# Kernel tuning notes

Hardware: AMD Instinct MI355X
Metric: run time of the kernel (lower is better)

Reference implementation:

```python
import jax, jax.numpy as jnp
import numpy as np

WS = (2, 7, 7)       # window size (d,h,w)
SS = (1, 3, 3)       # shift size
NH = 6               # num heads
EPS = 1e-5


def _layernorm(x, g, b):
    m = jnp.mean(x, axis=-1, keepdims=True)
    v = jnp.mean((x - m) ** 2, axis=-1, keepdims=True)
    return (x - m) * jax.lax.rsqrt(v + EPS) * g + b


def _window_partition(x, ws):
    # x: (B, D, H, W, C) -> (B*nW, N, C)
    B, D, H, W, C = x.shape
    x = x.reshape(B, D // ws[0], ws[0], H // ws[1], ws[1], W // ws[2], ws[2], C)
    x = x.transpose(0, 1, 3, 5, 2, 4, 6, 7)
    return x.reshape(-1, ws[0] * ws[1] * ws[2], C)


def _window_reverse(w, ws, B, D, H, W):
    # w: (B*nW, N, C) -> (B, D, H, W, C)
    C = w.shape[-1]
    x = w.reshape(B, D // ws[0], H // ws[1], W // ws[2], ws[0], ws[1], ws[2], C)
    x = x.transpose(0, 1, 4, 2, 5, 3, 6, 7)
    return x.reshape(B, D, H, W, C)


def _rel_pos_index(ws):
    coords = np.stack(np.meshgrid(np.arange(ws[0]), np.arange(ws[1]), np.arange(ws[2]), indexing='ij'))
    cf = coords.reshape(3, -1)                      # (3, N)
    rel = cf[:, :, None] - cf[:, None, :]           # (3, N, N)
    rel = rel.transpose(1, 2, 0).copy()             # (N, N, 3)
    rel[..., 0] += ws[0] - 1
    rel[..., 1] += ws[1] - 1
    rel[..., 2] += ws[2] - 1
    rel[..., 0] *= (2 * ws[1] - 1) * (2 * ws[2] - 1)
    rel[..., 1] *= 2 * ws[2] - 1
    return rel.sum(-1)                              # (N, N) int


def _compute_mask(Dp, Hp, Wp, ws, ss):
    img = np.zeros((1, Dp, Hp, Wp, 1), np.float32)
    cnt = 0
    for d in (slice(-ws[0]), slice(-ws[0], -ss[0]), slice(-ss[0], None)):
        for h in (slice(-ws[1]), slice(-ws[1], -ss[1]), slice(-ss[1], None)):
            for w in (slice(-ws[2]), slice(-ws[2], -ss[2]), slice(-ss[2], None)):
                img[:, d, h, w, :] = cnt
                cnt += 1
    mw = np.asarray(_window_partition(jnp.asarray(img), ws)).squeeze(-1)  # (nW, N)
    am = mw[:, None, :] - mw[:, :, None]
    return np.where(am != 0, -100.0, 0.0).astype(np.float32)


def setup_inputs() -> dict:
    key = jax.random.key(0)
    ks = jax.random.split(key, 8)
    B, D, H, W, C = 4, 8, 56, 56, 192
    hid = 4 * C
    tbl = (2 * WS[0] - 1) * (2 * WS[1] - 1) * (2 * WS[2] - 1)
    s = 0.02
    return {
        'x': jax.random.normal(ks[0], (B, D, H, W, C), jnp.float32),
        'mask_matrix': jnp.asarray(_compute_mask(D, H, W, WS, SS)),
        'norm1_g': jnp.ones((C,), jnp.float32),
        'norm1_b': jnp.zeros((C,), jnp.float32),
        'qkv_w': jax.random.normal(ks[1], (3 * C, C), jnp.float32) * s,
        'qkv_b': jnp.zeros((3 * C,), jnp.float32),
        'rpb_table': jax.random.normal(ks[2], (tbl, NH), jnp.float32) * s,
        'proj_w': jax.random.normal(ks[3], (C, C), jnp.float32) * s,
        'proj_b': jnp.zeros((C,), jnp.float32),
        'norm2_g': jnp.ones((C,), jnp.float32),
        'norm2_b': jnp.zeros((C,), jnp.float32),
        'fc1_w': jax.random.normal(ks[4], (hid, C), jnp.float32) * s,
        'fc1_b': jnp.zeros((hid,), jnp.float32),
        'fc2_w': jax.random.normal(ks[5], (C, hid), jnp.float32) * s,
        'fc2_b': jnp.zeros((C,), jnp.float32),
    }


def reference(x, mask_matrix, norm1_g, norm1_b, qkv_w, qkv_b, rpb_table,
              proj_w, proj_b, norm2_g, norm2_b, fc1_w, fc1_b, fc2_w, fc2_b):
    B, D, H, W, C = x.shape
    hd = C // NH
    scale = hd ** -0.5
    N = WS[0] * WS[1] * WS[2]
    rpi = _rel_pos_index(WS)  # constant (N, N)

    shortcut = x
    h = _layernorm(x, norm1_g, norm1_b)
    # cyclic shift (dims divisible by window, no padding needed)
    sx = jnp.roll(h, (-SS[0], -SS[1], -SS[2]), axis=(1, 2, 3))
    xw = _window_partition(sx, WS)                      # (B_, N, C)
    B_ = xw.shape[0]

    qkv = (xw @ qkv_w.T + qkv_b).reshape(B_, N, 3, NH, hd).transpose(2, 0, 3, 1, 4)
    q, k, v = qkv[0] * scale, qkv[1], qkv[2]            # (B_, NH, N, hd)
    attn = jnp.einsum('bhnd,bhmd->bhnm', q, k)          # (B_, NH, N, N)

    bias = rpb_table[rpi.reshape(-1)].reshape(N, N, NH).transpose(2, 0, 1)
    attn = attn + bias[None]

    nW = mask_matrix.shape[0]
    attn = attn.reshape(B_ // nW, nW, NH, N, N) + mask_matrix[None, :, None]
    attn = jax.nn.softmax(attn.reshape(B_, NH, N, N), axis=-1)

    out = jnp.einsum('bhnm,bhmd->bhnd', attn, v).swapaxes(1, 2).reshape(B_, N, C)
    out = out @ proj_w.T + proj_b

    sx = _window_reverse(out, WS, B, D, H, W)
    x1 = jnp.roll(sx, (SS[0], SS[1], SS[2]), axis=(1, 2, 3))

    x = shortcut + x1
    h2 = _layernorm(x, norm2_g, norm2_b)
    h2 = jax.nn.gelu(h2 @ fc1_w.T + fc1_b, approximate=False) @ fc2_w.T + fc2_b
    return x + h2
```

## Files before the change

kernel.cpp:

```cpp
#include <hip/hip_runtime.h>
#include <math.h>

typedef short short8 __attribute__((ext_vector_type(8)));
typedef __bf16 bf16x8 __attribute__((ext_vector_type(8)));
typedef float floatx4 __attribute__((ext_vector_type(4)));
typedef float f32x4 __attribute__((ext_vector_type(4)));
typedef unsigned short ushort;
typedef unsigned int uint;

#define NTOK 100352
#define CCH 192
#define NWIN 1024
#define NSEQ 98
#define NSEQP 112
#define NHEAD 6
#define HD 32
#define VSTR 136
#define PSTR 40

typedef const __attribute__((address_space(1))) uint guint_t;
typedef __attribute__((address_space(3))) uint luint_t;

__device__ __forceinline__ float bf2f(ushort u) {
    union { uint i; float f; } x; x.i = ((uint)u) << 16; return x.f;
}
__device__ __forceinline__ ushort f2bf(float f) {
    uint u = __float_as_uint(f);
    uint r = (u + 0x7FFFu + ((u >> 16) & 1u)) >> 16;
    return (ushort)r;
}
__device__ __forceinline__ uint pack2bf(float a, float b) {
    return (uint)f2bf(a) | ((uint)f2bf(b) << 16);
}
__device__ __forceinline__ float ldT(const void* p, size_t i, bool bf) {
    return bf ? bf2f(((const ushort*)p)[i]) : ((const float*)p)[i];
}

__global__ void detect_kernel(const uint* __restrict__ n1g, uint* __restrict__ flag) {
    if (threadIdx.x == 0) flag[0] = (n1g[0] == 0x3F800000u) ? 0u : 1u;
}

__global__ __launch_bounds__(256) void prepw_kernel(
    const void* __restrict__ src, ushort* __restrict__ dst,
    int K, int NT, const void* __restrict__ g,
    const uint* __restrict__ flagp, int total)
{
    const bool bf = (*flagp != 0u);
    int e = blockIdx.x * 256 + threadIdx.x;
    if (e >= total) return;
    int j = e / K, kk = e - j * K;
    int nt = j >> 6, r = j & 63;
    int kc = kk / 192; int k2 = kk - kc * 192;
    int ktc = k2 >> 5, c = k2 & 31;
    int ci = kc * (NT * 6) + nt * 6 + ktc;
    int byteoff = (ci << 12) + (((r << 6) + (c << 1)) ^ ((r & 7) << 4));
    float vv = ldT(src, e, bf);
    if (g) vv *= ldT(g, kk, bf);
    *(ushort*)((char*)dst + byteoff) = f2bf(vv);
}

__global__ __launch_bounds__(256) void prepmisc_kernel(
    const void* qkvb, const void* projb, const void* fc2b,
    const void* fc1b, const void* fc1w, const void* g2, const void* b2,
    float* __restrict__ FB, const uint* __restrict__ flagp)
{
    const bool bf = (*flagp != 0u);
    int j = blockIdx.x * 256 + threadIdx.x;
    if (j >= 768) return;
    if (j < 576) FB[j] = ldT(qkvb, j, bf);
    if (j < 192) { FB[576 + j] = ldT(projb, j, bf); FB[768 + j] = ldT(fc2b, j, bf); }
    float c1 = 0.f, c2 = 0.f;
    for (int kk = 0; kk < 192; ++kk) {
        float w = ldT(fc1w, (size_t)j * 192 + kk, bf);
        c1 = fmaf(w, ldT(g2, kk, bf), c1);
        c2 = fmaf(w, ldT(b2, kk, bf), c2);
    }
    FB[1728 + j] = c1;
    FB[960 + j]  = c2 + ldT(fc1b, j, bf);
}

__global__ __launch_bounds__(256) void prepTB_kernel(
    const void* __restrict__ rpb, const void* __restrict__ mask,
    float* __restrict__ TB, const uint* __restrict__ flagp)
{
    const bool bf = (*flagp != 0u);
    int i = blockIdx.x * 256 + threadIdx.x;
    if (i >= 8 * NHEAD * 7 * NSEQP * 16) return;
    int ky16 = i & 15; int t1 = i >> 4;
    int qy = t1 % NSEQP; int t2 = t1 / NSEQP;
    int kt = t2 % 7; int t3 = t2 / 7;
    int head = t3 % NHEAD; int combo = t3 / NHEAD;
    int ky = kt * 16 + ky16;
    int kcl = ky < 97 ? ky : 97, qcl = qy < 97 ? qy : 97;
    int md = kcl / 49, mr = kcl % 49; int mh = mr / 7, mw = mr % 7;
    int nd = qcl / 49, nr = qcl % 49; int nh = nr / 7, nw = nr % 7;
    int idx = (nd - md) * 169 + (nh - mh) * 13 + (nw - mw) + 253;
    float b = ldT(rpb, (size_t)idx * NHEAD + head, bf);
    int wrem = ((combo & 4) ? (3 << 6) : 0) | ((combo & 2) ? (7 << 3) : 0) | ((combo & 1) ? 7 : 0);
    float m = ldT(mask, (size_t)wrem * (NSEQ * NSEQ) + (size_t)kcl * NSEQ + qcl, bf);
    TB[i] = b + m;
}

__global__ __launch_bounds__(256) void ln1_kernel(
    const void* __restrict__ x, const void* __restrict__ g,
    const void* __restrict__ b, ushort* __restrict__ xw,
    const uint* __restrict__ flagp)
{
    const bool bf = (*flagp != 0u);
    int tid = blockIdx.x * 4 + (threadIdx.x >> 6);
    int lane = threadIdx.x & 63;
    int wi = tid / NSEQ, n = tid % NSEQ;
    int bb = wi >> 8; int rem = wi & 255;
    int wd = rem >> 6; int wh = (rem >> 3) & 7; int ww = rem & 7;
    int dz = n / 49; int r2 = n % 49; int hy = r2 / 7; int wx = r2 % 7;
    int dd = wd * 2 + dz, hh = wh * 7 + hy, w2 = ww * 7 + wx;
    int dsrc = (dd + 1) & 7;
    int hsrc = hh + 3; if (hsrc >= 56) hsrc -= 56;
    int wsrc = w2 + 3; if (wsrc >= 56) wsrc -= 56;
    size_t base = ((size_t)((bb * 8 + dsrc) * 56 + hsrc) * 56 + wsrc) * CCH;
    float v0 = ldT(x, base + lane, bf);
    float v1 = ldT(x, base + lane + 64, bf);
    float v2 = ldT(x, base + lane + 128, bf);
    float s = v0 + v1 + v2;
    float ss = v0 * v0 + v1 * v1 + v2 * v2;
    for (int o = 32; o > 0; o >>= 1) { s += __shfl_xor(s, o, 64); ss += __shfl_xor(ss, o, 64); }
    float mean = s * (1.f / 192.f);
    float var = ss * (1.f / 192.f) - mean * mean;
    float rstd = rsqrtf(var + 1e-5f);
    ushort* dst = xw + (size_t)tid * CCH;
    dst[lane]       = f2bf((v0 - mean) * rstd * ldT(g, lane, bf)       + ldT(b, lane, bf));
    dst[lane + 64]  = f2bf((v1 - mean) * rstd * ldT(g, lane + 64, bf)  + ldT(b, lane + 64, bf));
    dst[lane + 128] = f2bf((v2 - mean) * rstd * ldT(g, lane + 128, bf) + ldT(b, lane + 128, bf));
}

#define KSTEP(CI, KT, ACC) do {                                                     \
    const int ci_ = (CI);                                                           \
    if (ci_ + 1 < TOT) {                                                            \
        const ushort* s_ = WB + ((size_t)(ci_ + 1) << 11) + (t << 3);               \
        ushort* d_ = (ushort*)Bs + (((ci_ + 1) & 1) << 11) + (wave << 9);           \
        __builtin_amdgcn_global_load_lds((guint_t*)s_, (luint_t*)d_, 16, 0, 0);     \
        asm volatile("s_waitcnt vmcnt(1) lgkmcnt(0)" ::: "memory");                 \
    } else {                                                                        \
        asm volatile("s_waitcnt vmcnt(0) lgkmcnt(0)" ::: "memory");                 \
    }                                                                               \
    __builtin_amdgcn_s_barrier();                                                   \
    __builtin_amdgcn_sched_barrier(0);                                              \
    {                                                                               \
        const char* bb_ = (const char*)Bs + ((ci_ & 1) << 12);                      \
        const ushort* ak_ = As + (KT) * 2560;                                       \
        bf16x8 a0_ = __builtin_bit_cast(bf16x8, *(const short8*)(ak_ + rowA));      \
        bf16x8 a1_ = __builtin_bit_cast(bf16x8, *(const short8*)(ak_ + rowA + 640));\
        bf16x8 b0_ = __builtin_bit_cast(bf16x8, *(const short8*)(bb_ + bOff0));     \
        bf16x8 b1_ = __builtin_bit_cast(bf16x8, *(const short8*)(bb_ + bOff0 + 1024));\
        ACC[0][0] = __builtin_amdgcn_mfma_f32_16x16x32_bf16(a0_, b0_, ACC[0][0], 0, 0, 0); \
        ACC[0][1] = __builtin_amdgcn_mfma_f32_16x16x32_bf16(a0_, b1_, ACC[0][1], 0, 0, 0); \
        ACC[1][0] = __builtin_amdgcn_mfma_f32_16x16x32_bf16(a1_, b0_, ACC[1][0], 0, 0, 0); \
        ACC[1][1] = __builtin_amdgcn_mfma_f32_16x16x32_bf16(a1_, b1_, ACC[1][1], 0, 0, 0); \
    }                                                                               \
    __builtin_amdgcn_sched_barrier(0);                                              \
    __builtin_amdgcn_s_barrier();                                                   \
} while (0)

template <int MODE>
__global__ __launch_bounds__(256, 4) void gemm_kernel(
    const ushort* __restrict__ Abf, const float* __restrict__ Af,
    const float* __restrict__ stats, const ushort* __restrict__ WB,
    const float* __restrict__ bias, const float* __restrict__ c1p,
    ushort* __restrict__ o0, ushort* __restrict__ o1, ushort* __restrict__ o2,
    float* __restrict__ xnew, const void* __restrict__ xorig,
    const float* __restrict__ xnew_in, void* __restrict__ outAny,
    float* __restrict__ statsOut,
    const uint* __restrict__ flagp)
{
    constexpr int NT   = (MODE == 0) ? 9 : (MODE == 2) ? 12 : 3;
    constexpr int NKC  = (MODE == 3) ? 4 : 1;
    constexpr int TOT  = NKC * NT * 6;
    constexpr int KROW = (MODE == 3) ? 768 : 192;
    const bool bf = (*flagp != 0u);
    __shared__ alignas(16) ushort As[15360];
    __shared__ alignas(16) ushort Bs[4096];
    const int t = threadIdx.x, wave = t >> 6, lane = t & 63;
    const int q = lane >> 4, l15 = lane & 15;
    const int wr = wave >> 1, wc = wave & 1;
    const int m0 = blockIdx.x * 64;
    const int rowA  = (wr * 32 + l15) * 40 + q * 8;
    const int bOff0 = ((wc * 32 + l15) * 64 + q * 16) ^ ((l15 & 7) << 4);
    const int sr = t >> 2, scg = (t & 3) * 8;

    {
        const ushort* s0 = WB + (t << 3);
        ushort* d0 = (ushort*)Bs + (wave << 9);
        __builtin_amdgcn_global_load_lds((guint_t*)s0, (luint_t*)d0, 16, 0, 0);
    }

    auto stageA = [&](int kc) {
        ushort* dA = As + sr * 40 + scg;
        if constexpr (MODE == 2) {
            const float* arow = Af + (size_t)(m0 + sr) * 192 + scg;
#pragma unroll
            for (int kt = 0; kt < 6; ++kt) {
                f32x4 x0 = *(const f32x4*)(arow + kt * 32);
                f32x4 x1 = *(const f32x4*)(arow + kt * 32 + 4);
                short8 dd;
#pragma unroll
                for (int e2 = 0; e2 < 4; ++e2) {
                    dd[e2]     = (short)f2bf(x0[e2]);
                    dd[e2 + 4] = (short)f2bf(x1[e2]);
                }
                *(short8*)(dA + kt * 2560) = dd;
            }
        } else {
            const ushort* arow = Abf + (size_t)(m0 + sr) * KROW + kc * 192 + scg;
#pragma unroll
            for (int kt = 0; kt < 6; ++kt)
                *(short8*)(dA + kt * 2560) = *(const short8*)(arow + kt * 32);
        }
    };

    if constexpr (MODE == 3) {
        floatx4 acc3[3][2][2];
#pragma unroll
        for (int a3 = 0; a3 < 3; ++a3)
#pragma unroll
            for (int mi = 0; mi < 2; ++mi)
#pragma unroll
                for (int ni = 0; ni < 2; ++ni) acc3[a3][mi][ni] = (floatx4){0.f, 0.f, 0.f, 0.f};
        for (int kc = 0; kc < 4; ++kc) {
            stageA(kc);
#pragma unroll
            for (int nt = 0; nt < 3; ++nt)
#pragma unroll
                for (int kt = 0; kt < 6; ++kt)
                    KSTEP(kc * 18 + nt * 6 + kt, kt, acc3[nt]);
        }
#pragma unroll
        for (int nt = 0; nt < 3; ++nt)
#pragma unroll
        for (int mi = 0; mi < 2; ++mi)
#pragma unroll
        for (int rr = 0; rr < 4; ++rr) {
            int m = m0 + wr * 32 + mi * 16 + q * 4 + rr;
#pragma unroll
            for (int ni = 0; ni < 2; ++ni) {
                int j = nt * 64 + wc * 32 + ni * 16 + l15;
                float val = acc3[nt][mi][ni][rr] + bias[j];
                size_t oi = (size_t)m * CCH + j;
                float res = val + xnew_in[oi];
                if (bf) ((ushort*)outAny)[oi] = f2bf(res);
                else    ((float*)outAny)[oi]  = res;
            }
        }
    } else {
        stageA(0);
        float ssum[2][4] = {{0.f,0.f,0.f,0.f},{0.f,0.f,0.f,0.f}};
        float ssq[2][4]  = {{0.f,0.f,0.f,0.f},{0.f,0.f,0.f,0.f}};
        for (int nt = 0; nt < NT; ++nt) {
            floatx4 acc[2][2];
#pragma unroll
            for (int mi = 0; mi < 2; ++mi)
#pragma unroll
                for (int ni = 0; ni < 2; ++ni) acc[mi][ni] = (floatx4){0.f, 0.f, 0.f, 0.f};
#pragma unroll
            for (int kt = 0; kt < 6; ++kt) KSTEP(nt * 6 + kt, kt, acc);

            if constexpr (MODE == 0) {
#pragma unroll
                for (int mi = 0; mi < 2; ++mi)
#pragma unroll
                for (int rr = 0; rr < 4; ++rr) {
                    int m = m0 + wr * 32 + mi * 16 + q * 4 + rr;
                    int wi2 = m / NSEQ, nn = m - wi2 * NSEQ;
#pragma unroll
                    for (int ni = 0; ni < 2; ++ni) {
                        int j = nt * 64 + wc * 32 + ni * 16 + l15;
                        float val = acc[mi][ni][rr] + bias[j];
                        int which = j / 192, remj = j - which * 192;
                        int head = remj >> 5, dd = remj & 31;
                        size_t off = (((size_t)(wi2 * NHEAD + head)) * NSEQ + nn) * HD + dd;
                        if (which == 0)      o0[off] = f2bf(val * 0.17677669529663687f);
                        else if (which == 1) o1[off] = f2bf(val);
                        else                 o2[off] = f2bf(val);
                    }
                }
            } else if constexpr (MODE == 1) {
#pragma unroll
                for (int mi = 0; mi < 2; ++mi)
#pragma unroll
                for (int rr = 0; rr < 4; ++rr) {
                    int m = m0 + wr * 32 + mi * 16 + q * 4 + rr;
                    int wi2 = m / NSEQ, nn = m - wi2 * NSEQ;
                    int bb2 = wi2 >> 8; int remw = wi2 & 255;
                    int wd = remw >> 6, wh = (remw >> 3) & 7, ww = remw & 7;
                    int dz = nn / 49; int r2 = nn - dz * 49; int hy = r2 / 7, wx = r2 - hy * 7;
                    int dd2 = wd * 2 + dz, hh = wh * 7 + hy, w2 = ww * 7 + wx;
                    int df = (dd2 + 1) & 7;
                    int hf = hh + 3; if (hf >= 56) hf -= 56;
                    int wf = w2 + 3; if (wf >= 56) wf -= 56;
                    size_t rowb = ((size_t)((bb2 * 8 + df) * 56 + hf) * 56 + wf) * CCH;
#pragma unroll
                    for (int ni = 0; ni < 2; ++ni) {
                        int j = nt * 64 + wc * 32 + ni * 16 + l15;
                        size_t idx = rowb + j;
                        float res = ldT(xorig, idx, bf) + acc[mi][ni][rr] + bias[j];
                        xnew[idx] = res;
                        ssum[mi][rr] += res;
                        ssq[mi][rr]  += res * res;
                    }
                }
            } else {
#pragma unroll
                for (int mi = 0; mi < 2; ++mi)
#pragma unroll
                for (int rr = 0; rr < 4; ++rr) {
                    int m = m0 + wr * 32 + mi * 16 + q * 4 + rr;
                    float mean = stats[2 * m], rstd = stats[2 * m + 1];
#pragma unroll
                    for (int ni = 0; ni < 2; ++ni) {
                        int j = nt * 64 + wc * 32 + ni * 16 + l15;
                        float val = acc[mi][ni][rr] * rstd - mean * rstd * c1p[j] + bias[j];
                        float gl = 0.5f * val * (1.0f + erff(val * 0.70710678118654752f));
                        o0[(size_t)m * 768 + j] = f2bf(gl);
                    }
                }
            }
        }
        if constexpr (MODE == 1) {
#pragma unroll
            for (int mi = 0; mi < 2; ++mi)
#pragma unroll
            for (int rr = 0; rr < 4; ++rr) {
#pragma unroll
                for (int off = 1; off <= 8; off <<= 1) {
                    ssum[mi][rr] += __shfl_xor(ssum[mi][rr], off, 64);
                    ssq[mi][rr]  += __shfl_xor(ssq[mi][rr], off, 64);
                }
            }
            __syncthreads();
            float* sm = (float*)Bs;
            if (wc == 0 && l15 == 0) {
#pragma unroll
                for (int mi = 0; mi < 2; ++mi)
#pragma unroll
                for (int rr = 0; rr < 4; ++rr) {
                    int tl = wr * 32 + mi * 16 + q * 4 + rr;
                    sm[2 * tl] = ssum[mi][rr];
                    sm[2 * tl + 1] = ssq[mi][rr];
                }
            }
            __syncthreads();
            if (wc == 1 && l15 == 0) {
#pragma unroll
                for (int mi = 0; mi < 2; ++mi)
#pragma unroll
                for (int rr = 0; rr < 4; ++rr) {
                    int tl = wr * 32 + mi * 16 + q * 4 + rr;
                    float s  = sm[2 * tl] + ssum[mi][rr];
                    float s2 = sm[2 * tl + 1] + ssq[mi][rr];
                    float mean = s * (1.f / 192.f);
                    float var = s2 * (1.f / 192.f) - mean * mean;
                    int m = m0 + tl;
                    int wi2 = m / NSEQ, nn = m - wi2 * NSEQ;
                    int bb2 = wi2 >> 8; int remw = wi2 & 255;
                    int wd = remw >> 6, wh = (remw >> 3) & 7, ww = remw & 7;
                    int dz = nn / 49; int r2 = nn - dz * 49; int hy = r2 / 7, wx = r2 - hy * 7;
                    int dd2 = wd * 2 + dz, hh = wh * 7 + hy, w2 = ww * 7 + wx;
                    int df = (dd2 + 1) & 7;
                    int hf = hh + 3; if (hf >= 56) hf -= 56;
                    int wf = w2 + 3; if (wf >= 56) wf -= 56;
                    int spat = ((bb2 * 8 + df) * 56 + hf) * 56 + wf;
                    statsOut[2 * spat]     = mean;
                    statsOut[2 * spat + 1] = rsqrtf(var + 1e-5f);
                }
            }
        }
    }
}

__global__ __launch_bounds__(128, 4) void attn_kernel(
    const ushort* __restrict__ qg, const ushort* __restrict__ kg,
    const ushort* __restrict__ vg, const float* __restrict__ TB,
    ushort* __restrict__ out)
{
    __shared__ alignas(16) ushort Vt[32 * VSTR];
    __shared__ alignas(16) ushort Ps[NSEQP * PSTR];
    const int blk = blockIdx.x;
    const int wi = blk / NHEAD, head = blk - wi * NHEAD;
    const int tid = threadIdx.x;
    const int wave = tid >> 6, lane = tid & 63;
    const int q = lane >> 4, l15 = lane & 15;
    const size_t base = (size_t)blk * (NSEQ * HD);

    {
        const uint* vp = (const uint*)(vg + base);
        for (int i = 0; i < 13; ++i) {
            int e2 = i * 128 + tid;
            if (e2 < 1568) {
                uint w = vp[e2];
                int key = e2 >> 4, d = (e2 & 15) * 2;
                Vt[d * VSTR + key]       = (ushort)(w & 0xFFFFu);
                Vt[(d + 1) * VSTR + key] = (ushort)(w >> 16);
            }
        }
        for (int i = 0; i < 8; ++i) {
            int idx = i * 128 + tid;
            if (idx < 960) {
                int d = idx / 30, key = 98 + (idx - d * 30);
                Vt[d * VSTR + key] = 0;
            }
        }
    }

    const int ntBeg = wave ? 4 : 0;
    const int NTW   = wave ? 3 : 4;

    bf16x8 qf[4];
#pragma unroll
    for (int i = 0; i < 4; ++i)
        if (i < NTW)
            qf[i] = __builtin_bit_cast(bf16x8,
                *(const short8*)(qg + base + (size_t)((ntBeg + i) * 16 + l15) * HD + q * 8));

    const int wrem = wi & 255;
    const int combo = (((wrem >> 6) == 3) ? 4 : 0) | ((((wrem >> 3) & 7) == 7) ? 2 : 0)
                    | (((wrem & 7) == 7) ? 1 : 0);
    const float* bt = TB + (size_t)(combo * NHEAD + head) * (7 * NSEQP * 16);

    floatx4 oacc[2][4];
#pragma unroll
    for (int dt = 0; dt < 2; ++dt)
#pragma unroll
        for (int i = 0; i < 4; ++i) oacc[dt][i] = (floatx4){0.f, 0.f, 0.f, 0.f};
    float rs[4] = {0.f, 0.f, 0.f, 0.f};

    __syncthreads();

    for (int ks = 0; ks < 4; ++ks) {
#pragma unroll
        for (int h = 0; h < 2; ++h) {
            const int kt = ks * 2 + h;
            if (kt < 7) {
                bf16x8 kfr = __builtin_bit_cast(bf16x8,
                    *(const short8*)(kg + base + (size_t)(kt * 16 + l15) * HD + q * 8));
                floatx4 st[4];
#pragma unroll
                for (int i = 0; i < 4; ++i)
                    if (i < NTW)
                        st[i] = __builtin_amdgcn_mfma_f32_16x16x32_bf16(
                            kfr, qf[i], (floatx4){0.f, 0.f, 0.f, 0.f}, 0, 0, 0);
#pragma unroll
                for (int i = 0; i < 4; ++i) {
                    if (i >= NTW) continue;
                    const int qy = (ntBeg + i) * 16 + l15;
                    f32x4 bv = *(const f32x4*)(bt + ((size_t)kt * NSEQP + qy) * 16 + q * 4);
                    float p[4];
#pragma unroll
                    for (int r = 0; r < 4; ++r) {
                        float pe = __expf(st[i][r] + bv[r]);
                        if (kt == 6 && (q * 4 + r) >= 2) pe = 0.f;
                        p[r] = pe;
                    }
                    rs[i] += (p[0] + p[1]) + (p[2] + p[3]);
                    uint* pr = (uint*)(Ps + (size_t)qy * PSTR + h * 16 + q * 4);
                    pr[0] = pack2bf(p[0], p[1]);
                    pr[1] = pack2bf(p[2], p[3]);
                }
            } else {
#pragma unroll
                for (int i = 0; i < 4; ++i) {
                    if (i >= NTW) continue;
                    uint* z = (uint*)(Ps + (size_t)((ntBeg + i) * 16 + l15) * PSTR + 16 + q * 4);
                    z[0] = 0u; z[1] = 0u;
                }
            }
        }
        bf16x8 va[2];
#pragma unroll
        for (int dt = 0; dt < 2; ++dt)
            va[dt] = __builtin_bit_cast(bf16x8,
                *(const short8*)(Vt + (size_t)(dt * 16 + l15) * VSTR + ks * 32 + q * 8));
#pragma unroll
        for (int i = 0; i < 4; ++i) {
            if (i >= NTW) continue;
            bf16x8 pb = __builtin_bit_cast(bf16x8,
                *(const short8*)(Ps + (size_t)((ntBeg + i) * 16 + l15) * PSTR + q * 8));
            oacc[0][i] = __builtin_amdgcn_mfma_f32_16x16x32_bf16(va[0], pb, oacc[0][i], 0, 0, 0);
            oacc[1][i] = __builtin_amdgcn_mfma_f32_16x16x32_bf16(va[1], pb, oacc[1][i], 0, 0, 0);
        }
    }

#pragma unroll
    for (int i = 0; i < 4; ++i) {
        float r = rs[i];
        r += __shfl_xor(r, 16, 64);
        r += __shfl_xor(r, 32, 64);
        rs[i] = 1.f / r;
    }
#pragma unroll
    for (int i = 0; i < 4; ++i) {
        if (i >= NTW) continue;
        const int nt = ntBeg + i;
        const int qy = nt * 16 + l15;
        if (nt == 6 && l15 >= 2) continue;
        ushort* op = out + ((size_t)wi * NSEQ + qy) * CCH + head * HD;
        const float inv = rs[i];
#pragma unroll
        for (int dt = 0; dt < 2; ++dt) {
            const int d0 = dt * 16 + q * 4;
            *(uint*)(op + d0)     = pack2bf(oacc[dt][i][0] * inv, oacc[dt][i][1] * inv);
            *(uint*)(op + d0 + 2) = pack2bf(oacc[dt][i][2] * inv, oacc[dt][i][3] * inv);
        }
    }
}

extern "C" void kernel_launch(void* const* d_in, const int* in_sizes, int n_in,
                              void* d_out, int out_size, void* d_ws, size_t ws_size,
                              hipStream_t stream)
{
    const void* x     = d_in[0];
    const void* mask  = d_in[1];
    const void* n1g   = d_in[2];
    const void* n1b   = d_in[3];
    const void* qkvw  = d_in[4];
    const void* qkvb  = d_in[5];
    const void* rpb   = d_in[6];
    const void* projw = d_in[7];
    const void* projb = d_in[8];
    const void* n2g   = d_in[9];
    const void* n2b   = d_in[10];
    const void* fc1w  = d_in[11];
    const void* fc1b  = d_in[12];
    const void* fc2w  = d_in[13];
    const void* fc2b  = d_in[14];

    char* ws = (char*)d_ws;
    const size_t SZB = (size_t)NTOK * CCH * 2;
    ushort* xw     = (ushort*)(ws);
    ushort* q      = (ushort*)(ws + SZB);
    ushort* k      = (ushort*)(ws + 2 * SZB);
    ushort* v      = (ushort*)(ws + 3 * SZB);
    float*  xnew   = (float*)(ws + 4 * SZB);
    float*  stats  = (float*)(ws + 6 * SZB);
    uint*   flag   = (uint*)(ws + 6 * SZB + 802816);
    ushort* hidden = (ushort*)(ws);
    char*   blob   = ws + 6 * SZB + 802816 + 256;
    ushort* WQ = (ushort*)(blob);
    ushort* WP = (ushort*)(blob + 221184);
    ushort* W1 = (ushort*)(blob + 294912);
    ushort* W2 = (ushort*)(blob + 589824);
    float*  FB = (float*)(blob + 884736);
    float*  TB = (float*)(ws + 4 * SZB);

    detect_kernel<<<1, 64, 0, stream>>>((const uint*)n1g, flag);
    prepmisc_kernel<<<3, 256, 0, stream>>>(qkvb, projb, fc2b, fc1b, fc1w, n2g, n2b, FB, flag);
    prepTB_kernel<<<2352, 256, 0, stream>>>(rpb, mask, TB, flag);
    prepw_kernel<<<432, 256, 0, stream>>>(qkvw, WQ, 192, 9,  nullptr, flag, 110592);
    prepw_kernel<<<144, 256, 0, stream>>>(projw, WP, 192, 3,  nullptr, flag, 36864);
    prepw_kernel<<<576, 256, 0, stream>>>(fc1w,  W1, 192, 12, n2g,     flag, 147456);
    prepw_kernel<<<576, 256, 0, stream>>>(fc2w,  W2, 768, 3,  nullptr, flag, 147456);
    ln1_kernel<<<NTOK / 4, 256, 0, stream>>>(x, n1g, n1b, xw, flag);
    gemm_kernel<0><<<NTOK / 64, 256, 0, stream>>>(
        xw, nullptr, nullptr, WQ, FB, nullptr,
        q, k, v, nullptr, nullptr, nullptr, nullptr, nullptr, flag);
    attn_kernel<<<NWIN * NHEAD, 128, 0, stream>>>(q, k, v, TB, xw);
    gemm_kernel<1><<<NTOK / 64, 256, 0, stream>>>(
        xw, nullptr, nullptr, WP, FB + 576, nullptr,
        nullptr, nullptr, nullptr, xnew, x, nullptr, nullptr, stats, flag);
    gemm_kernel<2><<<NTOK / 64, 256, 0, stream>>>(
        nullptr, xnew, stats, W1, FB + 960, FB + 1728,
        hidden, nullptr, nullptr, nullptr, nullptr, nullptr, nullptr, nullptr, flag);
    gemm_kernel<3><<<NTOK / 64, 256, 0, stream>>>(
        hidden, nullptr, nullptr, W2, FB + 768, nullptr,
        nullptr, nullptr, nullptr, nullptr, nullptr, xnew, d_out, nullptr, flag);
}
```

Baseline: 672.5 us.

## Fuse FC1+GELU+FC2 MLP into one kernel keeping hidden tile in LDS

Replaces the separate FC1 and FC2 GEMM kernels with a single fc_kernel. It computes each 64-wide hidden slice with GELU into shared memory and immediately accumulates it into the FC2 output, so the 768-wide hidden activation never goes to global memory. The fc1/fc2 weights are interleaved into one blob in consumption order. The post-attention residual trunk is now stored as bf16 instead of fp32, which halves its traffic but adds rounding to the residual path. The fused kernel holds more accumulators and uses more LDS, so launch bounds drop to 3 blocks per CU.

After: 648.7 us. 3.5% less time.

```diff
diff --git a/kernel.cpp b/kernel.cpp
--- a/kernel.cpp
+++ b/kernel.cpp
@@ -42,20 +42,41 @@
 
 __global__ __launch_bounds__(256) void prepw_kernel(
     const void* __restrict__ src, ushort* __restrict__ dst,
-    int K, int NT, const void* __restrict__ g,
-    const uint* __restrict__ flagp, int total)
+    int K, const uint* __restrict__ flagp, int total)
 {
     const bool bf = (*flagp != 0u);
     int e = blockIdx.x * 256 + threadIdx.x;
     if (e >= total) return;
     int j = e / K, kk = e - j * K;
     int nt = j >> 6, r = j & 63;
-    int kc = kk / 192; int k2 = kk - kc * 192;
-    int ktc = k2 >> 5, c = k2 & 31;
-    int ci = kc * (NT * 6) + nt * 6 + ktc;
+    int ktc = kk >> 5, c = kk & 31;
+    int ci = nt * 6 + ktc;
     int byteoff = (ci << 12) + (((r << 6) + (c << 1)) ^ ((r & 7) << 4));
-    float vv = ldT(src, e, bf);
-    if (g) vv *= ldT(g, kk, bf);
+    *(ushort*)((char*)dst + byteoff) = f2bf(ldT(src, e, bf));
+}
+
+__global__ __launch_bounds__(256) void prepwf_kernel(
+    const void* __restrict__ w1, const void* __restrict__ w2,
+    const void* __restrict__ g2, ushort* __restrict__ dst,
+    const uint* __restrict__ flagp)
+{
+    const bool bf = (*flagp != 0u);
+    int e = blockIdx.x * 256 + threadIdx.x;
+    if (e >= 294912) return;
+    int ci, r, c; float vv;
+    if (e < 147456) {
+        int j = e / 192, kk = e - j * 192;
+        ci = (j >> 6) * 12 + (kk >> 5);
+        r = j & 63; c = kk & 31;
+        vv = ldT(w1, e, bf) * ldT(g2, kk, bf);
+    } else {
+        int e2 = e - 147456;
+        int j = e2 / 768, kk = e2 - j * 768;
+        ci = (kk >> 6) * 12 + 6 + (j >> 6) * 2 + ((kk >> 5) & 1);
+        r = j & 63; c = kk & 31;
+        vv = ldT(w2, e2, bf);
+    }
+    int byteoff = (ci << 12) + (((r << 6) + (c << 1)) ^ ((r & 7) << 4));
     *(ushort*)((char*)dst + byteoff) = f2bf(vv);
 }
 
@@ -133,7 +154,7 @@
     dst[lane + 128] = f2bf((v2 - mean) * rstd * ldT(g, lane + 128, bf) + ldT(b, lane + 128, bf));
 }
 
-#define KSTEP(CI, KT, ACC) do {                                                     \
+#define KSTEP(CI, AKP, ACC) do {                                                    \
     const int ci_ = (CI);                                                           \
     if (ci_ + 1 < TOT) {                                                            \
         const ushort* s_ = WB + ((size_t)(ci_ + 1) << 11) + (t << 3);               \
@@ -147,7 +168,7 @@
     __builtin_amdgcn_sched_barrier(0);                                              \
     {                                                                               \
         const char* bb_ = (const char*)Bs + ((ci_ & 1) << 12);                      \
-        const ushort* ak_ = As + (KT) * 2560;                                       \
+        const ushort* ak_ = (AKP);                                                  \
         bf16x8 a0_ = __builtin_bit_cast(bf16x8, *(const short8*)(ak_ + rowA));      \
         bf16x8 a1_ = __builtin_bit_cast(bf16x8, *(const short8*)(ak_ + rowA + 640));\
         bf16x8 b0_ = __builtin_bit_cast(bf16x8, *(const short8*)(bb_ + bOff0));     \
@@ -163,19 +184,14 @@
 
 template <int MODE>
 __global__ __launch_bounds__(256, 4) void gemm_kernel(
-    const ushort* __restrict__ Abf, const float* __restrict__ Af,
-    const float* __restrict__ stats, const ushort* __restrict__ WB,
-    const float* __restrict__ bias, const float* __restrict__ c1p,
+    const ushort* __restrict__ Abf, const ushort* __restrict__ WB,
+    const float* __restrict__ bias,
     ushort* __restrict__ o0, ushort* __restrict__ o1, ushort* __restrict__ o2,
-    float* __restrict__ xnew, const void* __restrict__ xorig,
-    const float* __restrict__ xnew_in, void* __restrict__ outAny,
-    float* __restrict__ statsOut,
-    const uint* __restrict__ flagp)
-{
-    constexpr int NT   = (MODE == 0) ? 9 : (MODE == 2) ? 12 : 3;
-    constexpr int NKC  = (MODE == 3) ? 4 : 1;
-    constexpr int TOT  = NKC * NT * 6;
-    constexpr int KROW = (MODE == 3) ? 768 : 192;
+    const void* __restrict__ xorig, ushort* __restrict__ xnewB,
+    float* __restrict__ statsOut, const uint* __restrict__ flagp)
+{
+    constexpr int NT  = (MODE == 0) ? 9 : 3;
+    constexpr int TOT = NT * 6;
     const bool bf = (*flagp != 0u);
     __shared__ alignas(16) ushort As[15360];
     __shared__ alignas(16) ushort Bs[4096];
@@ -192,186 +208,221 @@
         ushort* d0 = (ushort*)Bs + (wave << 9);
         __builtin_amdgcn_global_load_lds((guint_t*)s0, (luint_t*)d0, 16, 0, 0);
     }
-
-    auto stageA = [&](int kc) {
+    {
+        const ushort* arow = Abf + (size_t)(m0 + sr) * 192 + scg;
         ushort* dA = As + sr * 40 + scg;
-        if constexpr (MODE == 2) {
-            const float* arow = Af + (size_t)(m0 + sr) * 192 + scg;
-#pragma unroll
-            for (int kt = 0; kt < 6; ++kt) {
-                f32x4 x0 = *(const f32x4*)(arow + kt * 32);
-                f32x4 x1 = *(const f32x4*)(arow + kt * 32 + 4);
-                short8 dd;
-#pragma unroll
-                for (int e2 = 0; e2 < 4; ++e2) {
-                    dd[e2]     = (short)f2bf(x0[e2]);
-                    dd[e2 + 4] = (short)f2bf(x1[e2]);
+#pragma unroll
+        for (int kt = 0; kt < 6; ++kt)
+            *(short8*)(dA + kt * 2560) = *(const short8*)(arow + kt * 32);
+    }
+
+    float ssum[2][4] = {{0.f,0.f,0.f,0.f},{0.f,0.f,0.f,0.f}};
+    float ssq[2][4]  = {{0.f,0.f,0.f,0.f},{0.f,0.f,0.f,0.f}};
+    for (int nt = 0; nt < NT; ++nt) {
+        floatx4 acc[2][2];
+#pragma unroll
+        for (int mi = 0; mi < 2; ++mi)
+#pragma unroll
+            for (int ni = 0; ni < 2; ++ni) acc[mi][ni] = (floatx4){0.f, 0.f, 0.f, 0.f};
+#pragma unroll
+        for (int kt = 0; kt < 6; ++kt) KSTEP(nt * 6 + kt, As + kt * 2560, acc);
+
+        if constexpr (MODE == 0) {
+#pragma unroll
+            for (int mi = 0; mi < 2; ++mi)
+#pragma unroll
+            for (int rr = 0; rr < 4; ++rr) {
+                int m = m0 + wr * 32 + mi * 16 + q * 4 + rr;
+                int wi2 = m / NSEQ, nn = m - wi2 * NSEQ;
+#pragma unroll
+                for (int ni = 0; ni < 2; ++ni) {
+                    int j = nt * 64 + wc * 32 + ni * 16 + l15;
+                    float val = acc[mi][ni][rr] + bias[j];
+                    int which = j / 192, remj = j - which * 192;
+                    int head = remj >> 5, dd = remj & 31;
+                    size_t off = (((size_t)(wi2 * NHEAD + head)) * NSEQ + nn) * HD + dd;
+                    if (which == 0)      o0[off] = f2bf(val * 0.17677669529663687f);
+                    else if (which == 1) o1[off] = f2bf(val);
+                    else                 o2[off] = f2bf(val);
                 }
-                *(short8*)(dA + kt * 2560) = dd;
             }
         } else {
-            const ushort* arow = Abf + (size_t)(m0 + sr) * KROW + kc * 192 + scg;
-#pragma unroll
-            for (int kt = 0; kt < 6; ++kt)
-                *(short8*)(dA + kt * 2560) = *(const short8*)(arow + kt * 32);
-        }
-    };
-
-    if constexpr (MODE == 3) {
-        floatx4 acc3[3][2][2];
-#pragma unroll
-        for (int a3 = 0; a3 < 3; ++a3)
 #pragma unroll
             for (int mi = 0; mi < 2; ++mi)
 #pragma unroll
-                for (int ni = 0; ni < 2; ++ni) acc3[a3][mi][ni] = (floatx4){0.f, 0.f, 0.f, 0.f};
-        for (int kc = 0; kc < 4; ++kc) {
-            stageA(kc);
-#pragma unroll
-            for (int nt = 0; nt < 3; ++nt)
-#pragma unroll
-                for (int kt = 0; kt < 6; ++kt)
-                    KSTEP(kc * 18 + nt * 6 + kt, kt, acc3[nt]);
-        }
-#pragma unroll
-        for (int nt = 0; nt < 3; ++nt)
+            for (int rr = 0; rr < 4; ++rr) {
+                int m = m0 + wr * 32 + mi * 16 + q * 4 + rr;
+                int wi2 = m / NSEQ, nn = m - wi2 * NSEQ;
+                int bb2 = wi2 >> 8; int remw = wi2 & 255;
+                int wd = remw >> 6, wh = (remw >> 3) & 7, ww = remw & 7;
+                int dz = nn / 49; int r2 = nn - dz * 49; int hy = r2 / 7, wx = r2 - hy * 7;
+                int dd2 = wd * 2 + dz, hh = wh * 7 + hy, w2 = ww * 7 + wx;
+                int df = (dd2 + 1) & 7;
+                int hf = hh + 3; if (hf >= 56) hf -= 56;
+                int wf = w2 + 3; if (wf >= 56) wf -= 56;
+                size_t rowb = ((size_t)((bb2 * 8 + df) * 56 + hf) * 56 + wf) * CCH;
+#pragma unroll
+                for (int ni = 0; ni < 2; ++ni) {
+                    int j = nt * 64 + wc * 32 + ni * 16 + l15;
+                    size_t idx = rowb + j;
+                    float res = ldT(xorig, idx, bf) + acc[mi][ni][rr] + bias[j];
+                    xnewB[idx] = f2bf(res);
+                    ssum[mi][rr] += res;
+                    ssq[mi][rr]  += res * res;
+                }
+            }
+        }
+    }
+    if constexpr (MODE == 1) {
 #pragma unroll
         for (int mi = 0; mi < 2; ++mi)
 #pragma unroll
         for (int rr = 0; rr < 4; ++rr) {
-            int m = m0 + wr * 32 + mi * 16 + q * 4 + rr;
-#pragma unroll
-            for (int ni = 0; ni < 2; ++ni) {
-                int j = nt * 64 + wc * 32 + ni * 16 + l15;
-                float val = acc3[nt][mi][ni][rr] + bias[j];
-                size_t oi = (size_t)m * CCH + j;
-                float res = val + xnew_in[oi];
-                if (bf) ((ushort*)outAny)[oi] = f2bf(res);
-                else    ((float*)outAny)[oi]  = res;
-            }
-        }
-    } else {
-        stageA(0);
-        float ssum[2][4] = {{0.f,0.f,0.f,0.f},{0.f,0.f,0.f,0.f}};
-        float ssq[2][4]  = {{0.f,0.f,0.f,0.f},{0.f,0.f,0.f,0.f}};
-        for (int nt = 0; nt < NT; ++nt) {
-            floatx4 acc[2][2];
+#pragma unroll
+            for (int off = 1; off <= 8; off <<= 1) {
+                ssum[mi][rr] += __shfl_xor(ssum[mi][rr], off, 64);
+                ssq[mi][rr]  += __shfl_xor(ssq[mi][rr], off, 64);
+            }
+        }
+        __syncthreads();
+        float* sm = (float*)Bs;
+        if (wc == 0 && l15 == 0) {
 #pragma unroll
             for (int mi = 0; mi < 2; ++mi)
 #pragma unroll
-                for (int ni = 0; ni < 2; ++ni) acc[mi][ni] = (floatx4){0.f, 0.f, 0.f, 0.f};
-#pragma unroll
-            for (int kt = 0; kt < 6; ++kt) KSTEP(nt * 6 + kt, kt, acc);
-
-            if constexpr (MODE == 0) {
-#pragma unroll
-                for (int mi = 0; mi < 2; ++mi)
-#pragma unroll
-                for (int rr = 0; rr < 4; ++rr) {
-                    int m = m0 + wr * 32 + mi * 16 + q * 4 + rr;
-                    int wi2 = m / NSEQ, nn = m - wi2 * NSEQ;
-#pragma unroll
-                    for (int ni = 0; ni < 2; ++ni) {
-                        int j = nt * 64 + wc * 32 + ni * 16 + l15;
-                        float val = acc[mi][ni][rr] + bias[j];
-                        int which = j / 192, remj = j - which * 192;
-                        int head = remj >> 5, dd = remj & 31;
-                        size_t off = (((size_t)(wi2 * NHEAD + head)) * NSEQ + nn) * HD + dd;
-                        if (which == 0)      o0[off] = f2bf(val * 0.17677669529663687f);
-                        else if (which == 1) o1[off] = f2bf(val);
-                        else                 o2[off] = f2bf(val);
-                    }
-                }
-            } else if constexpr (MODE == 1) {
-#pragma unroll
-                for (int mi = 0; mi < 2; ++mi)
-#pragma unroll
-                for (int rr = 0; rr < 4; ++rr) {
-                    int m = m0 + wr * 32 + mi * 16 + q * 4 + rr;
-                    int wi2 = m / NSEQ, nn = m - wi2 * NSEQ;
-                    int bb2 = wi2 >> 8; int remw = wi2 & 255;
-                    int wd = remw >> 6, wh = (remw >> 3) & 7, ww = remw & 7;
-                    int dz = nn / 49; int r2 = nn - dz * 49; int hy = r2 / 7, wx = r2 - hy * 7;
-                    int dd2 = wd * 2 + dz, hh = wh * 7 + hy, w2 = ww * 7 + wx;
-                    int df = (dd2 + 1) & 7;
-                    int hf = hh + 3; if (hf >= 56) hf -= 56;
-                    int wf = w2 + 3; if (wf >= 56) wf -= 56;
-                    size_t rowb = ((size_t)((bb2 * 8 + df) * 56 + hf) * 56 + wf) * CCH;
-#pragma unroll
-                    for (int ni = 0; ni < 2; ++ni) {
-                        int j = nt * 64 + wc * 32 + ni * 16 + l15;
-                        size_t idx = rowb + j;
-                        float res = ldT(xorig, idx, bf) + acc[mi][ni][rr] + bias[j];
-                        xnew[idx] = res;
-                        ssum[mi][rr] += res;
-                        ssq[mi][rr]  += res * res;
-                    }
-                }
-            } else {
-#pragma unroll
-                for (int mi = 0; mi < 2; ++mi)
-#pragma unroll
-                for (int rr = 0; rr < 4; ++rr) {
-                    int m = m0 + wr * 32 + mi * 16 + q * 4 + rr;
-                    float mean = stats[2 * m], rstd = stats[2 * m + 1];
-#pragma unroll
-                    for (int ni = 0; ni < 2; ++ni) {
-                        int j = nt * 64 + wc * 32 + ni * 16 + l15;
-                        float val = acc[mi][ni][rr] * rstd - mean * rstd * c1p[j] + bias[j];
-                        float gl = 0.5f * val * (1.0f + erff(val * 0.70710678118654752f));
-                        o0[(size_t)m * 768 + j] = f2bf(gl);
-                    }
-                }
-            }
-        }
-        if constexpr (MODE == 1) {
+            for (int rr = 0; rr < 4; ++rr) {
+                int tl = wr * 32 + mi * 16 + q * 4 + rr;
+                sm[2 * tl] = ssum[mi][rr];
+                sm[2 * tl + 1] = ssq[mi][rr];
+            }
+        }
+        __syncthreads();
+        if (wc == 1 && l15 == 0) {
 #pragma unroll
             for (int mi = 0; mi < 2; ++mi)
 #pragma unroll
             for (int rr = 0; rr < 4; ++rr) {
-#pragma unroll
-                for (int off = 1; off <= 8; off <<= 1) {
-                    ssum[mi][rr] += __shfl_xor(ssum[mi][rr], off, 64);
-                    ssq[mi][rr]  += __shfl_xor(ssq[mi][rr], off, 64);
-                }
-            }
-            __syncthreads();
-            float* sm = (float*)Bs;
-            if (wc == 0 && l15 == 0) {
-#pragma unroll
-                for (int mi = 0; mi < 2; ++mi)
-#pragma unroll
-                for (int rr = 0; rr < 4; ++rr) {
-                    int tl = wr * 32 + mi * 16 + q * 4 + rr;
-                    sm[2 * tl] = ssum[mi][rr];
-                    sm[2 * tl + 1] = ssq[mi][rr];
-                }
-            }
-            __syncthreads();
-            if (wc == 1 && l15 == 0) {
-#pragma unroll
-                for (int mi = 0; mi < 2; ++mi)
-#pragma unroll
-                for (int rr = 0; rr < 4; ++rr) {
-                    int tl = wr * 32 + mi * 16 + q * 4 + rr;
-                    float s  = sm[2 * tl] + ssum[mi][rr];
-                    float s2 = sm[2 * tl + 1] + ssq[mi][rr];
-                    float mean = s * (1.f / 192.f);
-                    float var = s2 * (1.f / 192.f) - mean * mean;
-                    int m = m0 + tl;
-                    int wi2 = m / NSEQ, nn = m - wi2 * NSEQ;
-                    int bb2 = wi2 >> 8; int remw = wi2 & 255;
-                    int wd = remw >> 6, wh = (remw >> 3) & 7, ww = remw & 7;
-                    int dz = nn / 49; int r2 = nn - dz * 49; int hy = r2 / 7, wx = r2 - hy * 7;
-                    int dd2 = wd * 2 + dz, hh = wh * 7 + hy, w2 = ww * 7 + wx;
-                    int df = (dd2 + 1) & 7;
-                    int hf = hh + 3; if (hf >= 56) hf -= 56;
-                    int wf = w2 + 3; if (wf >= 56) wf -= 56;
-                    int spat = ((bb2 * 8 + df) * 56 + hf) * 56 + wf;
-                    statsOut[2 * spat]     = mean;
-                    statsOut[2 * spat + 1] = rsqrtf(var + 1e-5f);
-                }
-            }
+                int tl = wr * 32 + mi * 16 + q * 4 + rr;
+                float s  = sm[2 * tl] + ssum[mi][rr];
+                float s2 = sm[2 * tl + 1] + ssq[mi][rr];
+                float mean = s * (1.f / 192.f);
+                float var = s2 * (1.f / 192.f) - mean * mean;
+                int m = m0 + tl;
+                int wi2 = m / NSEQ, nn = m - wi2 * NSEQ;
+                int bb2 = wi2 >> 8; int remw = wi2 & 255;
+                int wd = remw >> 6, wh = (remw >> 3) & 7, ww = remw & 7;
+                int dz = nn / 49; int r2 = nn - dz * 49; int hy = r2 / 7, wx = r2 - hy * 7;
+                int dd2 = wd * 2 + dz, hh = wh * 7 + hy, w2 = ww * 7 + wx;
+                int df = (dd2 + 1) & 7;
+                int hf = hh + 3; if (hf >= 56) hf -= 56;
+                int wf = w2 + 3; if (wf >= 56) wf -= 56;
+                int spat = ((bb2 * 8 + df) * 56 + hf) * 56 + wf;
+                statsOut[2 * spat]     = mean;
+                statsOut[2 * spat + 1] = rsqrtf(var + 1e-5f);
+            }
+        }
+    }
+}
+
+__global__ __launch_bounds__(256, 3) void fc_kernel(
+    const ushort* __restrict__ trunk, const float* __restrict__ stats,
+    const ushort* __restrict__ WB, const float* __restrict__ cb,
+    const float* __restrict__ c1p, const float* __restrict__ f2b,
+    void* __restrict__ outAny, const uint* __restrict__ flagp)
+{
+    constexpr int TOT = 144;
+    const bool bf = (*flagp != 0u);
+    __shared__ alignas(16) ushort As[15360];
+    __shared__ alignas(16) ushort Hs[5120];
+    __shared__ alignas(16) ushort Bs[4096];
+    const int t = threadIdx.x, wave = t >> 6, lane = t & 63;
+    const int q = lane >> 4, l15 = lane & 15;
+    const int wr = wave >> 1, wc = wave & 1;
+    const int m0 = blockIdx.x * 64;
+    const int rowA  = (wr * 32 + l15) * 40 + q * 8;
+    const int bOff0 = ((wc * 32 + l15) * 64 + q * 16) ^ ((l15 & 7) << 4);
+    const int sr = t >> 2, scg = (t & 3) * 8;
+
+    {
+        const ushort* s0 = WB + (t << 3);
+        ushort* d0 = (ushort*)Bs + (wave << 9);
+        __builtin_amdgcn_global_load_lds((guint_t*)s0, (luint_t*)d0, 16, 0, 0);
+    }
+    {
+        const ushort* arow = trunk + (size_t)(m0 + sr) * 192 + scg;
+        ushort* dA = As + sr * 40 + scg;
+#pragma unroll
+        for (int kt = 0; kt < 6; ++kt)
+            *(short8*)(dA + kt * 2560) = *(const short8*)(arow + kt * 32);
+    }
+    float rstd_[2][4], mrs_[2][4];
+#pragma unroll
+    for (int mi = 0; mi < 2; ++mi)
+#pragma unroll
+    for (int rr = 0; rr < 4; ++rr) {
+        int m = m0 + wr * 32 + mi * 16 + q * 4 + rr;
+        float mean = stats[2 * m], rs = stats[2 * m + 1];
+        rstd_[mi][rr] = rs; mrs_[mi][rr] = mean * rs;
+    }
+
+    floatx4 f2a[3][2][2];
+#pragma unroll
+    for (int n3 = 0; n3 < 3; ++n3)
+#pragma unroll
+        for (int mi = 0; mi < 2; ++mi)
+#pragma unroll
+            for (int ni = 0; ni < 2; ++ni) f2a[n3][mi][ni] = (floatx4){0.f, 0.f, 0.f, 0.f};
+
+    for (int ht = 0; ht < 12; ++ht) {
+        floatx4 a1[2][2];
+#pragma unroll
+        for (int mi = 0; mi < 2; ++mi)
+#pragma unroll
+            for (int ni = 0; ni < 2; ++ni) a1[mi][ni] = (floatx4){0.f, 0.f, 0.f, 0.f};
+#pragma unroll
+        for (int kt = 0; kt < 6; ++kt) KSTEP(ht * 12 + kt, As + kt * 2560, a1);
+
+        float c1v0 = c1p[ht * 64 + wc * 32 + l15];
+        float c1v1 = c1p[ht * 64 + wc * 32 + 16 + l15];
+        float cbv0 = cb[ht * 64 + wc * 32 + l15];
+        float cbv1 = cb[ht * 64 + wc * 32 + 16 + l15];
+        ushort* hp = Hs + wc * 2560;
+#pragma unroll
+        for (int mi = 0; mi < 2; ++mi)
+#pragma unroll
+        for (int ni = 0; ni < 2; ++ni)
+#pragma unroll
+        for (int rr = 0; rr < 4; ++rr) {
+            float val = a1[mi][ni][rr] * rstd_[mi][rr]
+                      - mrs_[mi][rr] * (ni ? c1v1 : c1v0) + (ni ? cbv1 : cbv0);
+            float gl = 0.5f * val * (1.0f + erff(val * 0.70710678118654752f));
+            hp[(wr * 32 + mi * 16 + q * 4 + rr) * 40 + ni * 16 + l15] = f2bf(gl);
+        }
+        __syncthreads();
+#pragma unroll
+        for (int nt3 = 0; nt3 < 3; ++nt3)
+#pragma unroll
+            for (int kt2 = 0; kt2 < 2; ++kt2)
+                KSTEP(ht * 12 + 6 + nt3 * 2 + kt2, Hs + kt2 * 2560, f2a[nt3]);
+        __syncthreads();
+    }
+
+#pragma unroll
+    for (int nt3 = 0; nt3 < 3; ++nt3)
+#pragma unroll
+    for (int mi = 0; mi < 2; ++mi)
+#pragma unroll
+    for (int rr = 0; rr < 4; ++rr) {
+        int mrow = wr * 32 + mi * 16 + q * 4 + rr;
+        int m = m0 + mrow;
+#pragma unroll
+        for (int ni = 0; ni < 2; ++ni) {
+            int j = nt3 * 64 + wc * 32 + ni * 16 + l15;
+            float res = f2a[nt3][mi][ni][rr] + f2b[j]
+                      + bf2f(As[(j >> 5) * 2560 + mrow * 40 + (j & 31)]);
+            size_t oi = (size_t)m * CCH + j;
+            if (bf) ((ushort*)outAny)[oi] = f2bf(res);
+            else    ((float*)outAny)[oi]  = res;
         }
     }
 }
@@ -538,37 +589,28 @@
     ushort* q      = (ushort*)(ws + SZB);
     ushort* k      = (ushort*)(ws + 2 * SZB);
     ushort* v      = (ushort*)(ws + 3 * SZB);
-    float*  xnew   = (float*)(ws + 4 * SZB);
+    ushort* xnewB  = (ushort*)(ws + 4 * SZB);
+    float*  TB     = (float*)(ws + 5 * SZB);
     float*  stats  = (float*)(ws + 6 * SZB);
     uint*   flag   = (uint*)(ws + 6 * SZB + 802816);
-    ushort* hidden = (ushort*)(ws);
     char*   blob   = ws + 6 * SZB + 802816 + 256;
     ushort* WQ = (ushort*)(blob);
     ushort* WP = (ushort*)(blob + 221184);
-    ushort* W1 = (ushort*)(blob + 294912);
-    ushort* W2 = (ushort*)(blob + 589824);
+    ushort* WF = (ushort*)(blob + 294912);
     float*  FB = (float*)(blob + 884736);
-    float*  TB = (float*)(ws + 4 * SZB);
 
     detect_kernel<<<1, 64, 0, stream>>>((const uint*)n1g, flag);
     prepmisc_kernel<<<3, 256, 0, stream>>>(qkvb, projb, fc2b, fc1b, fc1w, n2g, n2b, FB, flag);
     prepTB_kernel<<<2352, 256, 0, stream>>>(rpb, mask, TB, flag);
-    prepw_kernel<<<432, 256, 0, stream>>>(qkvw, WQ, 192, 9,  nullptr, flag, 110592);
-    prepw_kernel<<<144, 256, 0, stream>>>(projw, WP, 192, 3,  nullptr, flag, 36864);
-    prepw_kernel<<<576, 256, 0, stream>>>(fc1w,  W1, 192, 12, n2g,     flag, 147456);
-    prepw_kernel<<<576, 256, 0, stream>>>(fc2w,  W2, 768, 3,  nullptr, flag, 147456);
+    prepw_kernel<<<432, 256, 0, stream>>>(qkvw, WQ, 192, flag, 110592);
+    prepw_kernel<<<144, 256, 0, stream>>>(projw, WP, 192, flag, 36864);
+    prepwf_kernel<<<1152, 256, 0, stream>>>(fc1w, fc2w, n2g, WF, flag);
     ln1_kernel<<<NTOK / 4, 256, 0, stream>>>(x, n1g, n1b, xw, flag);
     gemm_kernel<0><<<NTOK / 64, 256, 0, stream>>>(
-        xw, nullptr, nullptr, WQ, FB, nullptr,
-        q, k, v, nullptr, nullptr, nullptr, nullptr, nullptr, flag);
+        xw, WQ, FB, q, k, v, nullptr, nullptr, nullptr, flag);
     attn_kernel<<<NWIN * NHEAD, 128, 0, stream>>>(q, k, v, TB, xw);
     gemm_kernel<1><<<NTOK / 64, 256, 0, stream>>>(
-        xw, nullptr, nullptr, WP, FB + 576, nullptr,
-        nullptr, nullptr, nullptr, xnew, x, nullptr, nullptr, stats, flag);
-    gemm_kernel<2><<<NTOK / 64, 256, 0, stream>>>(
-        nullptr, xnew, stats, W1, FB + 960, FB + 1728,
-        hidden, nullptr, nullptr, nullptr, nullptr, nullptr, nullptr, nullptr, flag);
-    gemm_kernel<3><<<NTOK / 64, 256, 0, stream>>>(
-        hidden, nullptr, nullptr, W2, FB + 768, nullptr,
-        nullptr, nullptr, nullptr, nullptr, nullptr, xnew, d_out, nullptr, flag);
-}
+        xw, WP, FB + 576, nullptr, nullptr, nullptr, x, xnewB, stats, flag);
+    fc_kernel<<<NTOK / 64, 256, 0, stream>>>(
+        xnewB, stats, WF, FB + 960, FB + 1728, FB + 768, d_out, flag);
+}
```
